# Kernel optimization log

Measured on AMD Instinct MI355X. Metric: run time of the kernel, lower is better.

Reference implementation:

```python
import jax, jax.numpy as jnp
import numpy as np

D_MODEL = 1024

def setup_inputs() -> dict:
    key = jax.random.key(0)
    ks = jax.random.split(key, 7)
    B, S, D = 4, 2048, D_MODEL
    scale = 1.0 / np.sqrt(D)
    x = jax.random.normal(ks[0], (B, S, D), dtype=jnp.float32)
    Wq = jax.random.normal(ks[1], (D, D), dtype=jnp.float32) * scale
    bq = jnp.zeros((D,), dtype=jnp.float32)
    Wk = jax.random.normal(ks[2], (D, D), dtype=jnp.float32) * scale
    bk = jnp.zeros((D,), dtype=jnp.float32)
    Wv = jax.random.normal(ks[3], (D, D), dtype=jnp.float32) * scale
    bv = jnp.zeros((D,), dtype=jnp.float32)
    return {"x": x, "Wq": Wq, "bq": bq, "Wk": Wk, "bk": bk, "Wv": Wv, "bv": bv}

def reference(x, Wq, bq, Wk, bk, Wv, bv):
    # Single-head attention; scale = 1/sqrt(d_model) as in the torch module (self.d_k = d_model).
    d_k = x.shape[-1]
    q = jnp.einsum('bsd,de->bse', x, Wq) + bq
    k = jnp.einsum('bsd,de->bse', x, Wk) + bk
    v = jnp.einsum('bsd,de->bse', x, Wv) + bv
    scores = jnp.einsum('bqd,bkd->bqk', q, k) / jnp.sqrt(jnp.asarray(d_k, x.dtype))
    attn = jax.nn.softmax(scores, axis=-1)
    return jnp.einsum('bqk,bkd->bqd', attn, v)
```

## Files before the change

kernel.cpp:

```cpp
#include <hip/hip_runtime.h>
#include <hip/hip_bf16.h>

#define DM 1024
#define SEQ 2048
#define NBATCH 4

using f32x4 = __attribute__((ext_vector_type(4))) float;
using s16x8 = __attribute__((ext_vector_type(8))) short;
using u16x4 = __attribute__((ext_vector_type(4))) unsigned short;
using u16x8 = __attribute__((ext_vector_type(8))) unsigned short;

__device__ __forceinline__ unsigned short f2bf(float f) {
  union { float f; unsigned u; } v; v.f = f;
  return (unsigned short)((v.u + 0x7fffu + ((v.u >> 16) & 1u)) >> 16);
}

__global__ void prep_k(const float* __restrict__ X,
                       const float* __restrict__ Wq, const float* __restrict__ Wk,
                       const float* __restrict__ Wv,
                       unsigned short* __restrict__ XB, unsigned short* __restrict__ WT) {
  __shared__ float t[32][33];
  const int b = blockIdx.x;
  if (b < 4096) {
    const int i = b * 256 + threadIdx.x;
    const f32x4* p = (const f32x4*)X;
    f32x4 a = p[2 * i], c = p[2 * i + 1];
    u16x8 o;
#pragma unroll
    for (int q = 0; q < 4; q++) { o[q] = f2bf(a[q]); o[4 + q] = f2bf(c[q]); }
    *(u16x8*)(XB + (size_t)i * 8) = o;
  } else {
    const int r2 = b - 4096;
    const int seg = r2 >> 10;
    const int rem = r2 & 1023;
    const int k0 = (rem >> 5) * 32, n0 = (rem & 31) * 32;
    const float* W = (seg == 0) ? Wq : (seg == 1) ? Wk : Wv;
    unsigned short* out = WT + (size_t)seg * DM * DM;
    const int tr = threadIdx.x >> 5, tc = threadIdx.x & 31;
#pragma unroll
    for (int p = 0; p < 4; p++) {
      int r = tr + p * 8;
      t[r][tc] = W[(size_t)(k0 + r) * DM + n0 + tc];
    }
    __syncthreads();
#pragma unroll
    for (int p = 0; p < 4; p++) {
      int r = tr + p * 8;
      out[(size_t)(n0 + r) * DM + k0 + tc] = f2bf(t[tc][r]);
    }
  }
}

__global__ void combine_k(const float* __restrict__ ms, const float* __restrict__ ss,
                          float* __restrict__ T) {
  const int idx = blockIdx.x * 256 + threadIdx.x;
  const float* m = ms + (size_t)idx * 16;
  const float* s = ss + (size_t)idx * 32;
  float mv[16];
#pragma unroll
  for (int t = 0; t < 16; t++) mv[t] = m[t];
  float M = mv[0];
#pragma unroll
  for (int t = 1; t < 16; t++) M = fmaxf(M, mv[t]);
  float L = 0.f;
#pragma unroll
  for (int t = 0; t < 16; t++) L += (s[2 * t] + s[2 * t + 1]) * __expf(mv[t] - M);
  T[idx] = 1.0f;
#pragma unroll
  for (int t = 1; t < 16; t++) T[t * 8192 + idx] = __expf(mv[t - 1] - mv[t]);
  T[16 * 8192 + idx] = __expf(mv[15] - M) / L;
}

template <int MODE, int BM, int LDA, int LDB, int KDIM>
__global__ void gemm_nt(const unsigned short* __restrict__ A,
                        const unsigned short* __restrict__ B,
                        void* __restrict__ C0,
                        unsigned short* __restrict__ C1,
                        unsigned short* __restrict__ C2,
                        const float* __restrict__ bq,
                        const float* __restrict__ bk,
                        const float* __restrict__ bv,
                        float* __restrict__ sm,
                        float* __restrict__ sv,
                        const float* __restrict__ Tt) {
  constexpr int ASTEPS = BM / 32;
  constexpr int NJ = (BM == 128) ? 4 : 2;
  constexpr int WNOFF = 16 * NJ;
  __shared__ unsigned short lbuf[(BM + 128) * 64];
  __shared__ float fred[256];

  const int tid = threadIdx.x;
  const int w = tid >> 6;
  const int L = tid & 63;
  const int wm = (BM == 128) ? (w & 1) : 0;
  const int wn = (BM == 128) ? (w >> 1) : w;
  const int qd = L >> 4, ll = L & 15;

  const int bid = blockIdx.x;
  const int xcd = bid & 7, slot = bid >> 3;
  int bz, tileM, tileN, nT;
  if (MODE == 0) {
    const int pm = xcd & 3, pn = xcd >> 2;
    const int nloc = slot % 12, mloc = slot / 12;
    bz = 0; tileM = (pm * 16 + mloc) * 128; tileN = (pn * 12 + nloc) * 128; nT = 0;
  } else if (MODE == 1) {
    bz = xcd >> 1;
    const int mh = xcd & 1;
    const int nloc = slot & 15, mloc = slot >> 4;
    tileM = (mh * 8 + mloc) * 128; tileN = nloc * 128; nT = nloc;
  } else {
    bz = xcd >> 1;
    const int mh = xcd & 1;
    const int nloc = slot & 7, mloc = slot >> 3;
    tileM = (mh * 16 + mloc) * 64; tileN = nloc * 128; nT = nloc;
  }
  (void)nT;

  const unsigned short* Ab = A;
  const unsigned short* Bb = B;
  if (MODE == 1) { Ab += (size_t)bz * SEQ * DM; Bb += (size_t)bz * SEQ * DM; }
  if (MODE == 2) { Ab += (size_t)bz * SEQ * SEQ; Bb += (size_t)bz * DM * SEQ; }

  const int srow = tid >> 3;
  const int pch = tid & 7;
  const int gch = pch ^ (srow & 7);
  const unsigned short* gA = Ab + (size_t)(tileM + srow) * LDA + gch * 8;
  const unsigned short* gB = Bb + (size_t)(tileN + srow) * LDB + gch * 8;
  unsigned short* lA = lbuf;
  unsigned short* lB = lbuf + BM * 64;
  unsigned short* wAp = &lA[srow * 64 + pch * 8];
  unsigned short* wBp = &lB[srow * 64 + pch * 8];

  u16x8 rA[ASTEPS], rB[4];
#define LOADT(kt) do {                                                         \
    const size_t kk_ = (size_t)(kt) * 64;                                      \
    _Pragma("unroll")                                                          \
    for (int i_ = 0; i_ < ASTEPS; i_++)                                        \
      rA[i_] = *(const u16x8*)(gA + (size_t)i_ * 32 * LDA + kk_);              \
    _Pragma("unroll")                                                          \
    for (int i_ = 0; i_ < 4; i_++)                                             \
      rB[i_] = *(const u16x8*)(gB + (size_t)i_ * 32 * LDB + kk_);              \
  } while (0)
#define WRITET() do {                                                          \
    _Pragma("unroll")                                                          \
    for (int i_ = 0; i_ < ASTEPS; i_++) *(u16x8*)(wAp + i_ * 32 * 64) = rA[i_];\
    _Pragma("unroll")                                                          \
    for (int i_ = 0; i_ < 4; i_++)      *(u16x8*)(wBp + i_ * 32 * 64) = rB[i_];\
  } while (0)

  f32x4 acc[4][NJ];
#pragma unroll
  for (int i = 0; i < 4; i++)
#pragma unroll
    for (int j = 0; j < NJ; j++) acc[i][j] = (f32x4){0.f, 0.f, 0.f, 0.f};

  const int sw = L & 7;

  float tTn[4][4];
  const float* Tb = nullptr;
  if (MODE == 2) {
    Tb = Tt + (size_t)bz * SEQ + tileM;
#pragma unroll
    for (int i = 0; i < 4; i++)
#pragma unroll
      for (int r = 0; r < 4; r++) tTn[i][r] = Tb[1 * 8192 + i * 16 + qd * 4 + r];
  }

  constexpr int NK = KDIM / 64;
  LOADT(0);
  WRITET();
  __syncthreads();

  for (int k = 0; k < NK; ++k) {
    if (MODE == 2 && k >= 2 && (k & 1) == 0) {
#pragma unroll
      for (int i = 0; i < 4; i++)
#pragma unroll
        for (int j = 0; j < NJ; j++)
#pragma unroll
          for (int r = 0; r < 4; r++) acc[i][j][r] *= tTn[i][r];
      const int tn = (k >> 1) + 1;
#pragma unroll
      for (int i = 0; i < 4; i++)
#pragma unroll
        for (int r = 0; r < 4; r++) tTn[i][r] = Tb[(size_t)tn * 8192 + i * 16 + qd * 4 + r];
    }

    if (k + 1 < NK) LOADT(k + 1);

#pragma unroll
    for (int s = 0; s < 2; s++) {
      const int pc = ((s * 4 + qd) ^ sw) * 8;
      s16x8 av[4], bv4[NJ];
#pragma unroll
      for (int i = 0; i < 4; i++)
        av[i] = *(const s16x8*)&lA[(wm * 64 + i * 16 + ll) * 64 + pc];
#pragma unroll
      for (int j = 0; j < NJ; j++)
        bv4[j] = *(const s16x8*)&lB[(wn * WNOFF + j * 16 + ll) * 64 + pc];
#pragma unroll
      for (int i = 0; i < 4; i++)
#pragma unroll
        for (int j = 0; j < NJ; j++)
          acc[i][j] = __builtin_amdgcn_mfma_f32_16x16x32_bf16(av[i], bv4[j], acc[i][j], 0, 0, 0);
    }

    if (k + 1 < NK) {
      __builtin_amdgcn_s_waitcnt(0xC07F);
      __builtin_amdgcn_sched_barrier(0);
      __builtin_amdgcn_s_barrier();
      __builtin_amdgcn_sched_barrier(0);
      WRITET();
      __syncthreads();
    }
  }
#undef LOADT
#undef WRITET

  if (MODE == 0) {
#pragma unroll
    for (int i = 0; i < 4; i++) {
      const int gm0 = tileM + wm * 64 + i * 16 + qd * 4;
#pragma unroll
      for (int j = 0; j < NJ; j++) {
        const int gn = tileN + wn * WNOFF + j * 16 + ll;
        const int seg = gn >> 10;
        const int colin = gn & 1023;
        if (seg == 0) {
          const float bias = bq[colin];
          unsigned short* Q = (unsigned short*)C0;
#pragma unroll
          for (int r = 0; r < 4; r++) Q[(size_t)(gm0 + r) * DM + colin] = f2bf(acc[i][j][r] + bias);
        } else if (seg == 1) {
          const float bias = bk[colin];
#pragma unroll
          for (int r = 0; r < 4; r++) C1[(size_t)(gm0 + r) * DM + colin] = f2bf(acc[i][j][r] + bias);
        } else {
          const float bias = bv[colin];
          u16x4 pk;
#pragma unroll
          for (int r = 0; r < 4; r++) pk[r] = f2bf(acc[i][j][r] + bias);
          const int b = gm0 >> 11, s0 = gm0 & 2047;
          *(u16x4*)(C2 + ((size_t)((b << 10) + colin)) * SEQ + s0) = pk;
        }
      }
    }
  } else if (MODE == 1) {
    __syncthreads();
    float mt[4][4];
#pragma unroll
    for (int i = 0; i < 4; i++)
#pragma unroll
      for (int r = 0; r < 4; r++) {
#pragma unroll
        for (int j = 0; j < NJ; j++) acc[i][j][r] *= 0.03125f;
        float v = fmaxf(fmaxf(acc[i][0][r], acc[i][1][r]), fmaxf(acc[i][2][r], acc[i][3][r]));
#pragma unroll
        for (int m = 1; m < 16; m <<= 1) v = fmaxf(v, __shfl_xor(v, m, 16));
        mt[i][r] = v;
      }
    if (ll == 0) {
#pragma unroll
      for (int i = 0; i < 4; i++)
#pragma unroll
        for (int r = 0; r < 4; r++)
          fred[wn * 128 + wm * 64 + i * 16 + qd * 4 + r] = mt[i][r];
    }
    __syncthreads();
#pragma unroll
    for (int i = 0; i < 4; i++)
#pragma unroll
      for (int r = 0; r < 4; r++) {
        const int row = wm * 64 + i * 16 + qd * 4 + r;
        mt[i][r] = fmaxf(fred[row], fred[128 + row]);
      }
#pragma unroll
    for (int i = 0; i < 4; i++)
#pragma unroll
      for (int r = 0; r < 4; r++) {
        const int row = wm * 64 + i * 16 + qd * 4 + r;
        float s = 0.f;
#pragma unroll
        for (int j = 0; j < NJ; j++) {
          float e = __expf(acc[i][j][r] - mt[i][r]);
          s += e;
          const int col = wn * WNOFF + j * 16 + ll;
          lbuf[row * 128 + ((((col >> 4) ^ (row & 7)) << 4) | (col & 15))] = f2bf(e);
        }
#pragma unroll
        for (int m = 1; m < 16; m <<= 1) s += __shfl_xor(s, m, 16);
        if (ll == 0) {
          const size_t base = (size_t)bz * SEQ + tileM + row;
          sv[base * 32 + nT * 2 + wn] = s;
          if (wn == 0) sm[base * 16 + nT] = mt[i][r];
        }
      }
    __syncthreads();
    unsigned short* P = (unsigned short*)C0 + (size_t)bz * SEQ * SEQ;
#pragma unroll
    for (int p = 0; p < 8; p++) {
      const int c = p * 256 + tid;
      const int row = c >> 4, cg = c & 15;
      const int phys = ((((cg >> 1) ^ (row & 7)) << 4) | ((cg & 1) << 3));
      u16x8 val = *(const u16x8*)&lbuf[row * 128 + phys];
      *(u16x8*)(P + (size_t)(tileM + row) * SEQ + tileN + cg * 8) = val;
    }
  } else {
    float* O = (float*)C0 + (size_t)bz * SEQ * DM;
#pragma unroll
    for (int i = 0; i < 4; i++) {
      const int gm0 = tileM + i * 16 + qd * 4;
#pragma unroll
      for (int j = 0; j < NJ; j++) {
        const int gn = tileN + wn * WNOFF + j * 16 + ll;
#pragma unroll
        for (int r = 0; r < 4; r++)
          O[(size_t)(gm0 + r) * DM + gn] = acc[i][j][r] * tTn[i][r];
      }
    }
  }
}

extern "C" void kernel_launch(void* const* d_in, const int* in_sizes, int n_in,
                              void* d_out, int out_size, void* d_ws, size_t ws_size,
                              hipStream_t stream) {
  (void)in_sizes; (void)n_in; (void)out_size; (void)ws_size;
  const float* x  = (const float*)d_in[0];
  const float* Wq = (const float*)d_in[1];
  const float* bq = (const float*)d_in[2];
  const float* Wk = (const float*)d_in[3];
  const float* bk = (const float*)d_in[4];
  const float* Wv = (const float*)d_in[5];
  const float* bv = (const float*)d_in[6];
  float* out = (float*)d_out;
  char* ws = (char*)d_ws;
  unsigned short* xb = (unsigned short*)(ws + 0);
  unsigned short* wt = (unsigned short*)(ws + 16777216);
  unsigned short* qb = (unsigned short*)(ws + 23068672);
  unsigned short* kb = (unsigned short*)(ws + 39845888);
  unsigned short* vt = (unsigned short*)(ws + 56623104);
  unsigned short* P  = (unsigned short*)(ws + 73400320);
  float*          ms = (float*)(ws + 106954752);
  float*          ss = (float*)(ws + 107479040);
  float*          Tt = (float*)(ws + 108527616);

  prep_k<<<7168, 256, 0, stream>>>(x, Wq, Wk, Wv, xb, wt);
  gemm_nt<0, 128, 1024, 1024, 1024><<<1536, 256, 0, stream>>>(
      xb, wt, (void*)qb, kb, vt, bq, bk, bv, nullptr, nullptr, nullptr);
  gemm_nt<1, 128, 1024, 1024, 1024><<<1024, 256, 0, stream>>>(
      qb, kb, (void*)P, nullptr, nullptr, nullptr, nullptr, nullptr, ms, ss, nullptr);
  combine_k<<<32, 256, 0, stream>>>(ms, ss, Tt);
  gemm_nt<2, 64, 2048, 2048, 2048><<<1024, 256, 0, stream>>>(
      P, vt, (void*)out, nullptr, nullptr, nullptr, nullptr, nullptr, nullptr, nullptr, Tt);
}
```

Baseline: 248.3 us.

## Replace QKV projection GEMM with 256x256-tile kernel using direct global-to-LDS loads

Replaces the 128x128-tile MODE 0 GEMM for the fused QKV projection with a dedicated 512-thread kernel that computes 256x256 tiles. It streams A and B straight into LDS through a 4-stage ring of global_load_lds transfers, uses manual waitcnt and barriers to pipeline the loads, and raises wave priority around the MFMA blocks. The aim is more reuse per loaded byte and better overlap of memory traffic with MFMA work. In exchange it uses 128 KB of LDS and launches only 384 blocks, which lowers occupancy and may leave some CUs idle in the tail.

```diff
diff --git a/kernel.cpp b/kernel.cpp
--- a/kernel.cpp
+++ b/kernel.cpp
@@ -13,6 +13,12 @@
 __device__ __forceinline__ unsigned short f2bf(float f) {
   union { float f; unsigned u; } v; v.f = f;
   return (unsigned short)((v.u + 0x7fffu + ((v.u >> 16) & 1u)) >> 16);
+}
+
+__device__ __forceinline__ void gll16(const unsigned short* g, unsigned short* l) {
+  __builtin_amdgcn_global_load_lds((const __attribute__((address_space(1))) void*)g,
+                                   (__attribute__((address_space(3))) void*)l,
+                                   16, 0, 0);
 }
 
 __global__ void prep_k(const float* __restrict__ X,
@@ -69,6 +75,141 @@
 #pragma unroll
   for (int t = 1; t < 16; t++) T[t * 8192 + idx] = __expf(mv[t - 1] - mv[t]);
   T[16 * 8192 + idx] = __expf(mv[15] - M) / L;
+}
+
+__global__ __launch_bounds__(512, 2) void qkv8_k(
+    const unsigned short* __restrict__ A,
+    const unsigned short* __restrict__ B,
+    unsigned short* __restrict__ Qo, unsigned short* __restrict__ Ko,
+    unsigned short* __restrict__ Vt,
+    const float* __restrict__ bq, const float* __restrict__ bk,
+    const float* __restrict__ bv) {
+  constexpr int NKS = 32;
+  __shared__ unsigned short lds8[65536];
+  unsigned short* lA = lds8;
+  unsigned short* lB = lds8 + 32768;
+
+  const int tid = threadIdx.x;
+  const int w = tid >> 6, l = tid & 63;
+  const int ll = l & 15, qd = l >> 4;
+  const int wm = w & 1, wn = w >> 1;
+
+  const int bid = blockIdx.x;
+  const int xcd = bid & 7, slot = bid >> 3;
+  const int mt = xcd * 4 + slot / 12;
+  const int nt = slot % 12;
+  const int tileM = mt * 256, tileN = nt * 256;
+
+  const int seg = l >> 3, ch = l & 7;
+  const int rowo = seg * 2 + (ch >> 2);
+  const int kc = (ch & 3) ^ (seg & 3);
+  const unsigned short* gA0 = A + (size_t)(tileM + w * 16 + rowo) * DM + kc * 8;
+  const unsigned short* gA1 = gA0 + (size_t)128 * DM;
+  const unsigned short* gB0 = B + (size_t)(tileN + w * 16 + rowo) * DM + kc * 8;
+  const unsigned short* gB1 = gB0 + (size_t)128 * DM;
+  const int dA0 = w * 512, dA1 = (w + 8) * 512;
+
+#define STAGE_A(n_) do { unsigned short* d_ = lA + ((n_) & 3) * 8192;          \
+    gll16(gA0 + (size_t)(n_) * 32, d_ + dA0);                                  \
+    gll16(gA1 + (size_t)(n_) * 32, d_ + dA1); } while (0)
+#define STAGE_B(n_) do { unsigned short* d_ = lB + ((n_) & 3) * 8192;          \
+    gll16(gB0 + (size_t)(n_) * 32, d_ + dA0);                                  \
+    gll16(gB1 + (size_t)(n_) * 32, d_ + dA1); } while (0)
+
+  const int Ra = wm * 128 + ll;
+  const int aoff = (Ra >> 1) * 64 + ((Ra & 1) * 4 + (qd ^ ((Ra >> 1) & 3))) * 8;
+  const int Rb = wn * 64 + ll;
+  const int boff = (Rb >> 1) * 64 + ((Rb & 1) * 4 + (qd ^ ((Rb >> 1) & 3))) * 8;
+
+  f32x4 acc[8][4];
+#pragma unroll
+  for (int i = 0; i < 8; i++)
+#pragma unroll
+    for (int j = 0; j < 4; j++) acc[i][j] = (f32x4){0.f, 0.f, 0.f, 0.f};
+
+  STAGE_A(0); STAGE_B(0); STAGE_A(1); STAGE_B(1); STAGE_A(2); STAGE_B(2); STAGE_B(3);
+  __builtin_amdgcn_sched_barrier(0);
+  __builtin_amdgcn_s_waitcnt(0x0F7A);
+  __builtin_amdgcn_sched_barrier(0);
+  __builtin_amdgcn_s_barrier();
+  __builtin_amdgcn_sched_barrier(0);
+
+  for (int n = 0; n < NKS; ++n) {
+    const unsigned short* sA = lA + (n & 3) * 8192;
+    const unsigned short* sB = lB + (n & 3) * 8192;
+    s16x8 af[4], bf[4];
+
+#pragma unroll
+    for (int i = 0; i < 4; i++) af[i] = *(const s16x8*)&sA[aoff + i * 512];
+#pragma unroll
+    for (int j = 0; j < 4; j++) bf[j] = *(const s16x8*)&sB[boff + j * 512];
+    if (n + 3 < NKS) STAGE_A(n + 3);
+    __builtin_amdgcn_sched_barrier(0);
+    __builtin_amdgcn_s_barrier();
+    __builtin_amdgcn_s_waitcnt(0xC07F);
+    __builtin_amdgcn_sched_barrier(0);
+    __builtin_amdgcn_s_setprio(1);
+#pragma unroll
+    for (int i = 0; i < 4; i++)
+#pragma unroll
+      for (int j = 0; j < 4; j++)
+        acc[i][j] = __builtin_amdgcn_mfma_f32_16x16x32_bf16(af[i], bf[j], acc[i][j], 0, 0, 0);
+    __builtin_amdgcn_s_setprio(0);
+    __builtin_amdgcn_sched_barrier(0);
+    __builtin_amdgcn_s_barrier();
+    __builtin_amdgcn_sched_barrier(0);
+
+#pragma unroll
+    for (int i = 0; i < 4; i++) af[i] = *(const s16x8*)&sA[aoff + (i + 4) * 512];
+    if (n + 4 < NKS) STAGE_B(n + 4);
+    __builtin_amdgcn_sched_barrier(0);
+    __builtin_amdgcn_s_barrier();
+    __builtin_amdgcn_s_waitcnt(0xC07F);
+    __builtin_amdgcn_sched_barrier(0);
+    __builtin_amdgcn_s_setprio(1);
+#pragma unroll
+    for (int i = 0; i < 4; i++)
+#pragma unroll
+      for (int j = 0; j < 4; j++)
+        acc[i + 4][j] = __builtin_amdgcn_mfma_f32_16x16x32_bf16(af[i], bf[j], acc[i + 4][j], 0, 0, 0);
+    __builtin_amdgcn_s_setprio(0);
+    if (n < NKS - 4)       __builtin_amdgcn_s_waitcnt(0x0F7A);
+    else if (n == NKS - 4) __builtin_amdgcn_s_waitcnt(0x0F78);
+    else if (n == NKS - 3) __builtin_amdgcn_s_waitcnt(0x0F74);
+    else if (n == NKS - 2) __builtin_amdgcn_s_waitcnt(0x0F70);
+    __builtin_amdgcn_sched_barrier(0);
+    __builtin_amdgcn_s_barrier();
+    __builtin_amdgcn_sched_barrier(0);
+  }
+#undef STAGE_A
+#undef STAGE_B
+
+#pragma unroll
+  for (int i = 0; i < 8; i++) {
+    const int gm0 = tileM + wm * 128 + i * 16 + qd * 4;
+#pragma unroll
+    for (int j = 0; j < 4; j++) {
+      const int gn = tileN + wn * 64 + j * 16 + ll;
+      const int seg2 = gn >> 10;
+      const int colin = gn & 1023;
+      if (seg2 == 0) {
+        const float bias = bq[colin];
+#pragma unroll
+        for (int r = 0; r < 4; r++) Qo[(size_t)(gm0 + r) * DM + colin] = f2bf(acc[i][j][r] + bias);
+      } else if (seg2 == 1) {
+        const float bias = bk[colin];
+#pragma unroll
+        for (int r = 0; r < 4; r++) Ko[(size_t)(gm0 + r) * DM + colin] = f2bf(acc[i][j][r] + bias);
+      } else {
+        const float bias = bv[colin];
+        u16x4 pk;
+#pragma unroll
+        for (int r = 0; r < 4; r++) pk[r] = f2bf(acc[i][j][r] + bias);
+        const int b = gm0 >> 11, s0 = gm0 & 2047;
+        *(u16x4*)(Vt + ((size_t)((b << 10) + colin)) * SEQ + s0) = pk;
+      }
+    }
+  }
 }
 
 template <int MODE, int BM, int LDA, int LDB, int KDIM>
@@ -99,11 +240,7 @@
   const int bid = blockIdx.x;
   const int xcd = bid & 7, slot = bid >> 3;
   int bz, tileM, tileN, nT;
-  if (MODE == 0) {
-    const int pm = xcd & 3, pn = xcd >> 2;
-    const int nloc = slot % 12, mloc = slot / 12;
-    bz = 0; tileM = (pm * 16 + mloc) * 128; tileN = (pn * 12 + nloc) * 128; nT = 0;
-  } else if (MODE == 1) {
+  if (MODE == 1) {
     bz = xcd >> 1;
     const int mh = xcd & 1;
     const int nloc = slot & 15, mloc = slot >> 4;
@@ -217,35 +354,7 @@
 #undef LOADT
 #undef WRITET
 
-  if (MODE == 0) {
-#pragma unroll
-    for (int i = 0; i < 4; i++) {
-      const int gm0 = tileM + wm * 64 + i * 16 + qd * 4;
-#pragma unroll
-      for (int j = 0; j < NJ; j++) {
-        const int gn = tileN + wn * WNOFF + j * 16 + ll;
-        const int seg = gn >> 10;
-        const int colin = gn & 1023;
-        if (seg == 0) {
-          const float bias = bq[colin];
-          unsigned short* Q = (unsigned short*)C0;
-#pragma unroll
-          for (int r = 0; r < 4; r++) Q[(size_t)(gm0 + r) * DM + colin] = f2bf(acc[i][j][r] + bias);
-        } else if (seg == 1) {
-          const float bias = bk[colin];
-#pragma unroll
-          for (int r = 0; r < 4; r++) C1[(size_t)(gm0 + r) * DM + colin] = f2bf(acc[i][j][r] + bias);
-        } else {
-          const float bias = bv[colin];
-          u16x4 pk;
-#pragma unroll
-          for (int r = 0; r < 4; r++) pk[r] = f2bf(acc[i][j][r] + bias);
-          const int b = gm0 >> 11, s0 = gm0 & 2047;
-          *(u16x4*)(C2 + ((size_t)((b << 10) + colin)) * SEQ + s0) = pk;
-        }
-      }
-    }
-  } else if (MODE == 1) {
+  if (MODE == 1) {
     __syncthreads();
     float mt[4][4];
 #pragma unroll
@@ -305,7 +414,7 @@
       u16x8 val = *(const u16x8*)&lbuf[row * 128 + phys];
       *(u16x8*)(P + (size_t)(tileM + row) * SEQ + tileN + cg * 8) = val;
     }
-  } else {
+  } else if (MODE == 2) {
     float* O = (float*)C0 + (size_t)bz * SEQ * DM;
 #pragma unroll
     for (int i = 0; i < 4; i++) {
@@ -319,6 +428,7 @@
       }
     }
   }
+  (void)bq; (void)bk; (void)bv; (void)C1; (void)C2;
 }
 
 extern "C" void kernel_launch(void* const* d_in, const int* in_sizes, int n_in,
@@ -345,8 +455,7 @@
   float*          Tt = (float*)(ws + 108527616);
 
   prep_k<<<7168, 256, 0, stream>>>(x, Wq, Wk, Wv, xb, wt);
-  gemm_nt<0, 128, 1024, 1024, 1024><<<1536, 256, 0, stream>>>(
-      xb, wt, (void*)qb, kb, vt, bq, bk, bv, nullptr, nullptr, nullptr);
+  qkv8_k<<<384, 512, 0, stream>>>(xb, wt, qb, kb, vt, bq, bk, bv);
   gemm_nt<1, 128, 1024, 1024, 1024><<<1024, 256, 0, stream>>>(
       qb, kb, (void*)P, nullptr, nullptr, nullptr, nullptr, nullptr, ms, ss, nullptr);
   combine_k<<<32, 256, 0, stream>>>(ms, ss, Tt);
```

New measurement: 271.4 us. 9.3% more time.
